# Performance work log

Measured on AMD Instinct MI355X. Metric: run time of the kernel, lower is better.

Reference implementation:

```python
import jax, jax.numpy as jnp
import numpy as np

B = 131072      # batch
IN = 1024       # input_dim
H = 384         # hidden[0]
L = 128         # latent_dim = hidden[1]
K = 32          # slots_k
R = 2           # top_r
TAU = 0.7


def setup_inputs() -> dict:
    key = jax.random.key(0)
    ks = jax.random.split(key, 8)
    s = 0.02
    f32 = jnp.float32
    return {
        "x":  jax.random.normal(ks[0], (B, IN), f32),
        "w1": jax.random.normal(ks[1], (IN, H), f32) * s,
        "b1": jnp.zeros((H,), f32),
        "w2": jax.random.normal(ks[2], (H, L), f32) * s,
        "b2": jnp.zeros((L,), f32),
        "mk": jax.random.normal(ks[3], (K, L), f32) * s,  # memory_keys
        "mv": jax.random.normal(ks[4], (K, L), f32) * s,  # memory_values
        "w3": jax.random.normal(ks[5], (2 * L, H), f32) * s,
        "b3": jnp.zeros((H,), f32),
        "w4": jax.random.normal(ks[6], (H, 1), f32) * s,
        "b4": jnp.zeros((1,), f32),
    }


def reference(x, w1, b1, w2, b2, mk, mv, w3, b3, w4, b4):
    # block_a: Linear -> GELU -> (Dropout=id in eval) -> Linear -> GELU
    z = jax.nn.gelu(x @ w1 + b1, approximate=False)
    z = jax.nn.gelu(z @ w2 + b2, approximate=False)          # [B, L]

    # top-r slot attention over memory bank
    logits = (z @ mk.T) / TAU                                 # [B, K]
    _, idx = jax.lax.top_k(logits, R)                         # [B, R]
    keep = jax.nn.one_hot(idx, K, dtype=logits.dtype).sum(-2) > 0  # [B, K] bool
    masked = jnp.where(keep, logits, -jnp.inf)
    attn = jax.nn.softmax(masked, axis=-1)                    # [B, K]
    mem = attn @ mv                                           # [B, L]

    fused = jnp.concatenate([z, mem], axis=-1)                # [B, 2L]

    # default head: Linear -> GELU -> Linear(.,1)
    h = jax.nn.gelu(fused @ w3 + b3, approximate=False)
    logit = (h @ w4 + b4)[..., 0]                             # [B]
    return jax.nn.sigmoid(logit)
```

## Files before the change

### kernel.cpp

```cpp
#include <hip/hip_runtime.h>

#define BATCH   131072
#define INDIM   1024
#define BM      64
#define BDIM    512
#define NBLK    (BATCH / BM)

#define WT_OFF   0
#define XT0_OFF  98304
#define XT1_OFF  114688
#define Z1_OFF   0
#define W2T0_OFF 50176
#define W2T1_OFF 58368
#define FZ_OFF   0
#define RP_OFF   33792
#define W3T0_OFF 42240
#define W3T1_OFF 66816
#define CB_OFF   131072
#define B1S_OFF  (CB_OFF)
#define B2S_OFF  (CB_OFF + 1536)
#define B3S_OFF  (CB_OFF + 2048)
#define W4S_OFF  (CB_OFF + 3584)
#define MKS_OFF  (CB_OFF + 5120)
#define SMEM_BYTES (CB_OFF + 13824)

typedef unsigned short u16;
typedef u16    u16x8  __attribute__((ext_vector_type(8)));
typedef u16    u16x4  __attribute__((ext_vector_type(4)));
typedef __bf16 bf16x8 __attribute__((ext_vector_type(8)));
typedef __bf16 bf16x4 __attribute__((ext_vector_type(4)));
typedef float  f32x4  __attribute__((ext_vector_type(4)));

__device__ __forceinline__ u16 f2bf(float f) {
  unsigned u = __float_as_uint(f);
  u += 0x7FFFu + ((u >> 16) & 1u);
  return (u16)(u >> 16);
}

__device__ __forceinline__ float gelu_fast(float v) {
  float t = v * v;
  float u = v * fmaf(t, 0.0356774081f, 0.7978845608f);
  float e = __builtin_amdgcn_exp2f(u * -2.885390082f);
  return v * __builtin_amdgcn_rcpf(1.0f + e);
}

__device__ __forceinline__ f32x4 mfma16(u16x8 a, u16x8 b, f32x4 c) {
  return __builtin_amdgcn_mfma_f32_16x16x32_bf16(
      __builtin_bit_cast(bf16x8, a), __builtin_bit_cast(bf16x8, b), c, 0, 0, 0);
}

__device__ __forceinline__ u16x8 cvt8(float4 a, float4 b) {
  bf16x8 r;
  r[0]=(__bf16)a.x; r[1]=(__bf16)a.y; r[2]=(__bf16)a.z; r[3]=(__bf16)a.w;
  r[4]=(__bf16)b.x; r[5]=(__bf16)b.y; r[6]=(__bf16)b.z; r[7]=(__bf16)b.w;
  return __builtin_bit_cast(u16x8, r);
}
__device__ __forceinline__ u16x4 cvt4(float4 a) {
  bf16x4 r;
  r[0]=(__bf16)a.x; r[1]=(__bf16)a.y; r[2]=(__bf16)a.z; r[3]=(__bf16)a.w;
  return __builtin_bit_cast(u16x4, r);
}

typedef __attribute__((address_space(3))) unsigned int       lds_u32;
typedef __attribute__((address_space(1))) const unsigned int glb_u32;
__device__ __forceinline__ void gload16(const void* g, void* l) {
  __builtin_amdgcn_global_load_lds((glb_u32*)g, (lds_u32*)l, 16, 0, 0);
}

#define FENCE_SCHED __builtin_amdgcn_sched_barrier(0)
#define SOFT_LGKM0 asm volatile("s_waitcnt lgkmcnt(0)" ::: "memory")
#define SOFT_VMN(N) asm volatile("s_waitcnt vmcnt(" #N ")" ::: "memory")
#define BARRIER_LGKM do { \
  asm volatile("s_waitcnt lgkmcnt(0)" ::: "memory"); \
  __builtin_amdgcn_s_barrier(); FENCE_SCHED; } while (0)

__global__ void prep_kernel(const float* __restrict__ w1, const float* __restrict__ w2,
                            const float* __restrict__ w3, u16* __restrict__ w1s,
                            u16* __restrict__ w2s, u16* __restrict__ w3s) {
  int i = blockIdx.x * 256 + threadIdx.x;
  if (i < 393216) {
    int t = i / 49152, p = i % 49152;
    int r = p >> 7, q = p & 127, cp = q >> 3, o = q & 7;
    int cs = (cp & 8) | ((cp ^ (r & 7)) & 7);
    int k = t * 128 + cs * 8 + o;
    w1s[i] = f2bf(w1[k * 384 + r]);
  } else if (i < 442368) {
    int j = i - 393216;
    int t = j / 4096, p = j % 4096;
    int r = p >> 5, q = p & 31, cp = q >> 3, o = q & 7;
    int k = t * 32 + ((cp ^ ((r >> 1) & 3)) << 3) + o;
    w2s[j] = f2bf(w2[k * 128 + r]);
  } else if (i < 540672) {
    int j = i - 442368;
    int t = j / 12288, p = j % 12288;
    int r = p >> 5, q = p & 31, cp = q >> 3, o = q & 7;
    int k = t * 32 + ((cp ^ ((r >> 1) & 3)) << 3) + o;
    w3s[j] = f2bf(w3[k * 384 + r]);
  }
}

__global__ __launch_bounds__(BDIM, 2) void fused_kernel(
    const float* __restrict__ x,  const u16* __restrict__ w1s,
    const float* __restrict__ b1, const u16* __restrict__ w2s,
    const float* __restrict__ b2, const float* __restrict__ mkw,
    const float* __restrict__ mvw, const u16* __restrict__ w3s,
    const float* __restrict__ b3, const float* __restrict__ w4,
    const float* __restrict__ b4, float* __restrict__ out) {
  extern __shared__ char smem[];
  u16*   z1  = (u16*)(smem + Z1_OFF);
  u16*   fz  = (u16*)(smem + FZ_OFF);
  float* b1s = (float*)(smem + B1S_OFF);
  float* b2s = (float*)(smem + B2S_OFF);
  float* b3s = (float*)(smem + B3S_OFF);
  float* w4s = (float*)(smem + W4S_OFF);
  u16*   mks = (u16*)(smem + MKS_OFF);
  float* rowpart = (float*)(smem + RP_OFF);

  const int tid  = threadIdx.x;
  const int lane = tid & 63;
  const int wid  = tid >> 6;
  const int l15  = lane & 15;
  const int g    = lane >> 4;
  const int swz4 = (l15 >> 1) & 3;
  const int row0 = blockIdx.x * BM;
  const int wrow = wid * 48;
  const int wstrip = wid * 6144;

  {
    const u16* ws = w1s + wstrip + lane * 8;
    u16* wd = (u16*)(smem + WT_OFF) + wstrip;
    #pragma unroll
    for (int i = 0; i < 12; ++i) gload16(ws + i * 512, wd + i * 512);
  }
  FENCE_SCHED;
  const int xrow = tid >> 3, xq = tid & 7;
  const float* xp = x + (long)(row0 + xrow) * INDIM + xq * 16;
  const int c0 = 2 * xq, c1 = 2 * xq + 1;
  const int s0 = ((c0 & 8) | ((c0 ^ (xrow & 7)) & 7)) * 8;
  const int s1 = ((c1 & 8) | ((c1 ^ (xrow & 7)) & 7)) * 8;
  float4 xa0 = *(const float4*)xp,        xa1 = *(const float4*)(xp + 4);
  float4 xb0 = *(const float4*)(xp + 8),  xb1 = *(const float4*)(xp + 12);

  if (tid < 384) b1s[tid] = b1[tid];
  if (tid < 128) b2s[tid] = b2[tid];
  if (tid < 384) b3s[tid] = b3[tid];
  if (tid < 384) w4s[tid] = w4[tid];
  {
    int r = tid >> 4, cc = (tid & 15) * 8;
    const float4* pm = (const float4*)(mkw + r * 128 + cc);
    *(u16x8*)(mks + r * 136 + cc) = cvt8(pm[0], pm[1]);
  }
  {
    u16* xb = (u16*)(smem + XT0_OFF) + xrow * 128;
    *(u16x8*)(xb + s0) = cvt8(xa0, xa1);
    *(u16x8*)(xb + s1) = cvt8(xb0, xb1);
  }
  {
    const float* p = xp + 128;
    xa0 = *(const float4*)p;       xa1 = *(const float4*)(p + 4);
    xb0 = *(const float4*)(p + 8); xb1 = *(const float4*)(p + 12);
  }
  BARRIER_LGKM;

  f32x4 acc[4][3];
  #pragma unroll
  for (int m = 0; m < 4; ++m)
    #pragma unroll
    for (int n = 0; n < 3; ++n) acc[m][n] = (f32x4){0.f, 0.f, 0.f, 0.f};

  const u16* wtb = (const u16*)(smem + WT_OFF);
  for (int kt = 0; kt < 8; ++kt) {
    if (kt < 7) { SOFT_VMN(4); } else { SOFT_VMN(0); }
    const u16* xtb = (const u16*)(smem + ((kt & 1) ? XT1_OFF : XT0_OFF));
    #pragma unroll
    for (int s = 0; s < 4; ++s) {
      const int c = s * 4 + g;
      const int cs = ((c & 8) | ((c ^ (l15 & 7)) & 7)) * 8;
      u16x8 af[4], bfr[3];
      #pragma unroll
      for (int m = 0; m < 4; ++m) af[m] = *(const u16x8*)(xtb + (m * 16 + l15) * 128 + cs);
      #pragma unroll
      for (int n = 0; n < 3; ++n) bfr[n] = *(const u16x8*)(wtb + (wrow + n * 16 + l15) * 128 + cs);
      #pragma unroll
      for (int m = 0; m < 4; ++m)
        #pragma unroll
        for (int n = 0; n < 3; ++n) acc[m][n] = mfma16(bfr[n], af[m], acc[m][n]);
    }
    SOFT_LGKM0;
    if (kt < 7) {
      {
        const u16* ws = w1s + (kt + 1) * 49152 + wstrip + lane * 8;
        u16* wd = (u16*)(smem + WT_OFF) + wstrip;
        #pragma unroll
        for (int i = 0; i < 12; ++i) gload16(ws + i * 512, wd + i * 512);
      }
      {
        u16* xb = (u16*)(smem + ((kt & 1) ? XT0_OFF : XT1_OFF)) + xrow * 128;
        *(u16x8*)(xb + s0) = cvt8(xa0, xa1);
        *(u16x8*)(xb + s1) = cvt8(xb0, xb1);
      }
      if (kt < 6) {
        const float* p = xp + (kt + 2) * 128;
        xa0 = *(const float4*)p;       xa1 = *(const float4*)(p + 4);
        xb0 = *(const float4*)(p + 8); xb1 = *(const float4*)(p + 12);
      }
    }
    BARRIER_LGKM;
  }

  {
    const u16* s2 = w2s + wid * 512 + lane * 8;
    gload16(s2, (u16*)(smem + W2T0_OFF) + wid * 512);
    const u16* s2b = w2s + 4096 + wid * 512 + lane * 8;
    gload16(s2b, (u16*)(smem + W2T1_OFF) + wid * 512);
  }
  #pragma unroll
  for (int m = 0; m < 4; ++m) {
    #pragma unroll
    for (int n = 0; n < 3; ++n) {
      int col = wrow + n * 16 + g * 4;
      float4 bv = *(const float4*)(b1s + col);
      f32x4 a = acc[m][n];
      float4 gv = {gelu_fast(a[0] + bv.x), gelu_fast(a[1] + bv.y),
                   gelu_fast(a[2] + bv.z), gelu_fast(a[3] + bv.w)};
      *(u16x4*)(z1 + (m * 16 + l15) * 392 + col) = cvt4(gv);
    }
  }
  BARRIER_LGKM;

  f32x4 acc2[4];
  #pragma unroll
  for (int m = 0; m < 4; ++m) acc2[m] = (f32x4){0.f, 0.f, 0.f, 0.f};
  for (int kt = 0; kt < 12; ++kt) {
    if (kt < 11) { SOFT_VMN(1); } else { SOFT_VMN(0); }
    const u16* wb = (const u16*)(smem + ((kt & 1) ? W2T1_OFF : W2T0_OFF));
    u16x8 a2f[4];
    #pragma unroll
    for (int m = 0; m < 4; ++m)
      a2f[m] = *(const u16x8*)(z1 + (m * 16 + l15) * 392 + kt * 32 + g * 8);
    u16x8 b2f = *(const u16x8*)(wb + (wid * 16 + l15) * 32 + (g ^ swz4) * 8);
    SOFT_LGKM0;
    if (kt < 10) {
      const u16* s2 = w2s + (kt + 2) * 4096 + wid * 512 + lane * 8;
      gload16(s2, (u16*)(smem + ((kt & 1) ? W2T1_OFF : W2T0_OFF)) + wid * 512);
    }
    #pragma unroll
    for (int m = 0; m < 4; ++m) acc2[m] = mfma16(b2f, a2f[m], acc2[m]);
  }
  BARRIER_LGKM;

  {
    const u16* s3 = w3s + wid * 1536 + lane * 8;
    u16* d3 = (u16*)(smem + W3T0_OFF) + wid * 1536;
    gload16(s3, d3); gload16(s3 + 512, d3 + 512); gload16(s3 + 1024, d3 + 1024);
    const u16* s3b = w3s + 12288 + wid * 1536 + lane * 8;
    u16* d3b = (u16*)(smem + W3T1_OFF) + wid * 1536;
    gload16(s3b, d3b); gload16(s3b + 512, d3b + 512); gload16(s3b + 1024, d3b + 1024);
  }
  #pragma unroll
  for (int m = 0; m < 4; ++m) {
    int col = wid * 16 + g * 4;
    float4 bv = *(const float4*)(b2s + col);
    f32x4 a = acc2[m];
    float4 gv = {gelu_fast(a[0] + bv.x), gelu_fast(a[1] + bv.y),
                 gelu_fast(a[2] + bv.z), gelu_fast(a[3] + bv.w)};
    *(u16x4*)(fz + (m * 16 + l15) * 264 + col) = cvt4(gv);
  }
  BARRIER_LGKM;

  if (wid < 4) {
    const int wr = wid * 16 + l15;
    f32x4 accl[2] = {(f32x4){0,0,0,0}, (f32x4){0,0,0,0}};
    #pragma unroll
    for (int ks = 0; ks < 4; ++ks) {
      u16x8 afz = *(const u16x8*)(fz + wr * 264 + ks * 32 + g * 8);
      u16x8 k0  = *(const u16x8*)(mks + l15 * 136 + ks * 32 + g * 8);
      u16x8 k1  = *(const u16x8*)(mks + (16 + l15) * 136 + ks * 32 + g * 8);
      accl[0] = mfma16(k0, afz, accl[0]);
      accl[1] = mfma16(k1, afz, accl[1]);
    }
    float m1 = -3.4e38f, m2 = -3.4e38f; int i1 = -1, i2 = -1;
    #pragma unroll
    for (int n = 0; n < 2; ++n)
      #pragma unroll
      for (int j = 0; j < 4; ++j) {
        float v = accl[n][j]; int idx = n * 16 + g * 4 + j;
        if (v > m1) { m2 = m1; i2 = i1; m1 = v; i1 = idx; }
        else if (v > m2) { m2 = v; i2 = idx; }
      }
    #pragma unroll
    for (int d = 16; d <= 32; d <<= 1) {
      float om1 = __shfl_xor(m1, d); int oi1 = __shfl_xor(i1, d);
      float om2 = __shfl_xor(m2, d); int oi2 = __shfl_xor(i2, d);
      bool take = (om1 > m1) || (om1 == m1 && oi1 < i1);
      if (take) {
        float nm2; int ni2;
        if (m1 > om2 || (m1 == om2 && i1 < oi2)) { nm2 = m1; ni2 = i1; }
        else { nm2 = om2; ni2 = oi2; }
        m1 = om1; i1 = oi1; m2 = nm2; i2 = ni2;
      } else {
        if (om1 > m2 || (om1 == m2 && oi1 < i2)) { m2 = om1; i2 = oi1; }
      }
    }
    float a1 = __builtin_amdgcn_rcpf(
        1.0f + __builtin_amdgcn_exp2f((m2 - m1) * (1.44269504f / 0.7f)));
    float a2 = 1.0f - a1;
    const float* v1 = mvw + i1 * 128 + g * 32;
    const float* v2 = mvw + i2 * 128 + g * 32;
    #pragma unroll
    for (int c = 0; c < 4; ++c) {
      float4 A0 = *(const float4*)(v1 + c * 8), A1 = *(const float4*)(v1 + c * 8 + 4);
      float4 B0 = *(const float4*)(v2 + c * 8), B1 = *(const float4*)(v2 + c * 8 + 4);
      float4 r0 = {a1*A0.x + a2*B0.x, a1*A0.y + a2*B0.y, a1*A0.z + a2*B0.z, a1*A0.w + a2*B0.w};
      float4 r1 = {a1*A1.x + a2*B1.x, a1*A1.y + a2*B1.y, a1*A1.z + a2*B1.z, a1*A1.w + a2*B1.w};
      *(u16x8*)(fz + wr * 264 + 128 + g * 32 + c * 8) = cvt8(r0, r1);
    }
  }
  BARRIER_LGKM;

  f32x4 acc3[4][3];
  #pragma unroll
  for (int m = 0; m < 4; ++m)
    #pragma unroll
    for (int n = 0; n < 3; ++n) acc3[m][n] = (f32x4){0.f, 0.f, 0.f, 0.f};
  for (int kt = 0; kt < 8; ++kt) {
    if (kt < 7) { SOFT_VMN(3); } else { SOFT_VMN(0); }
    const u16* wb = (const u16*)(smem + ((kt & 1) ? W3T1_OFF : W3T0_OFF));
    u16x8 a3f[4], b3f[3];
    #pragma unroll
    for (int m = 0; m < 4; ++m)
      a3f[m] = *(const u16x8*)(fz + (m * 16 + l15) * 264 + kt * 32 + g * 8);
    #pragma unroll
    for (int n = 0; n < 3; ++n)
      b3f[n] = *(const u16x8*)(wb + (wrow + n * 16 + l15) * 32 + (g ^ swz4) * 8);
    SOFT_LGKM0;
    if (kt < 6) {
      const u16* s3 = w3s + (kt + 2) * 12288 + wid * 1536 + lane * 8;
      u16* d3 = (u16*)(smem + ((kt & 1) ? W3T1_OFF : W3T0_OFF)) + wid * 1536;
      gload16(s3, d3); gload16(s3 + 512, d3 + 512); gload16(s3 + 1024, d3 + 1024);
    }
    #pragma unroll
    for (int m = 0; m < 4; ++m)
      #pragma unroll
      for (int n = 0; n < 3; ++n) acc3[m][n] = mfma16(b3f[n], a3f[m], acc3[m][n]);
  }

  #pragma unroll
  for (int m = 0; m < 4; ++m) {
    float s = 0.f;
    #pragma unroll
    for (int n = 0; n < 3; ++n) {
      int col = wrow + n * 16 + g * 4;
      float4 bv = *(const float4*)(b3s + col);
      float4 wv = *(const float4*)(w4s + col);
      f32x4 a = acc3[m][n];
      s += gelu_fast(a[0] + bv.x) * wv.x + gelu_fast(a[1] + bv.y) * wv.y +
           gelu_fast(a[2] + bv.z) * wv.z + gelu_fast(a[3] + bv.w) * wv.w;
    }
    s += __shfl_xor(s, 16);
    s += __shfl_xor(s, 32);
    if (lane < 16) rowpart[(m * 16 + l15) * 8 + wid] = s;
  }
  BARRIER_LGKM;
  if (tid < BM) {
    const float4* rp = (const float4*)(rowpart + tid * 8);
    float4 p0 = rp[0], p1 = rp[1];
    float lg = b4[0] + p0.x + p0.y + p0.z + p0.w + p1.x + p1.y + p1.z + p1.w;
    out[row0 + tid] = __builtin_amdgcn_rcpf(1.0f + __builtin_amdgcn_exp2f(-lg * 1.44269504f));
  }
}

extern "C" void kernel_launch(void* const* d_in, const int* in_sizes, int n_in,
                              void* d_out, int out_size, void* d_ws, size_t ws_size,
                              hipStream_t stream) {
  const float* x  = (const float*)d_in[0];
  const float* w1 = (const float*)d_in[1];
  const float* b1 = (const float*)d_in[2];
  const float* w2 = (const float*)d_in[3];
  const float* b2 = (const float*)d_in[4];
  const float* mk = (const float*)d_in[5];
  const float* mv = (const float*)d_in[6];
  const float* w3 = (const float*)d_in[7];
  const float* b3 = (const float*)d_in[8];
  const float* w4 = (const float*)d_in[9];
  const float* b4 = (const float*)d_in[10];

  u16* w1s = (u16*)d_ws;
  u16* w2s = w1s + 393216;
  u16* w3s = w1s + 442368;

  prep_kernel<<<2112, 256, 0, stream>>>(w1, w2, w3, w1s, w2s, w3s);

  (void)hipFuncSetAttribute(reinterpret_cast<const void*>(fused_kernel),
                            hipFuncAttributeMaxDynamicSharedMemorySize, SMEM_BYTES);
  fused_kernel<<<NBLK, BDIM, SMEM_BYTES, stream>>>(x, w1s, b1, w2s, b2, mk, mv, w3s,
                                                   b3, w4, b4, (float*)d_out);
}
```

Before: 279.7 us.

## Double batch tile to 128 rows with 2x4 wave grid and double-buffered W1

Raises the per-block row tile from 64 to 128 and splits the 8 waves into a 2x4 grid for the first GEMM, so each wave computes 64 rows by 96 columns. The W1 weight tile is cut to 64-wide K slices that are double-buffered in LDS, and the barrier sits mid-iteration so the next slice's loads overlap the MFMAs. The aim is to halve how often each block reloads the weights per row and to improve compute-to-load ratio. In exchange, accumulator register pressure doubles (24 plus 24 f32x4 tiles), which may hurt occupancy at 2 blocks/CU, and half as many blocks are launched.

```diff
diff --git a/kernel.cpp b/kernel.cpp
--- a/kernel.cpp
+++ b/kernel.cpp
@@ -2,20 +2,21 @@
 
 #define BATCH   131072
 #define INDIM   1024
-#define BM      64
+#define BM      128
 #define BDIM    512
 #define NBLK    (BATCH / BM)
 
-#define WT_OFF   0
+#define WT0_OFF  0
+#define WT1_OFF  49152
 #define XT0_OFF  98304
 #define XT1_OFF  114688
 #define Z1_OFF   0
-#define W2T0_OFF 50176
-#define W2T1_OFF 58368
+#define W2T0_OFF 100352
+#define W2T1_OFF 108544
 #define FZ_OFF   0
-#define RP_OFF   33792
-#define W3T0_OFF 42240
-#define W3T1_OFF 66816
+#define W3T0_OFF 67584
+#define W3T1_OFF 92160
+#define RP_OFF   116736
 #define CB_OFF   131072
 #define B1S_OFF  (CB_OFF)
 #define B2S_OFF  (CB_OFF + 1536)
@@ -79,10 +80,9 @@
                             u16* __restrict__ w2s, u16* __restrict__ w3s) {
   int i = blockIdx.x * 256 + threadIdx.x;
   if (i < 393216) {
-    int t = i / 49152, p = i % 49152;
-    int r = p >> 7, q = p & 127, cp = q >> 3, o = q & 7;
-    int cs = (cp & 8) | ((cp ^ (r & 7)) & 7);
-    int k = t * 128 + cs * 8 + o;
+    int t = i / 24576, p = i % 24576;
+    int r = p >> 6, q = p & 63, cp = q >> 3, o = q & 7;
+    int k = t * 64 + ((cp ^ (r & 7)) << 3) + o;
     w1s[i] = f2bf(w1[k * 384 + r]);
   } else if (i < 442368) {
     int j = i - 393216;
@@ -121,25 +121,32 @@
   const int wid  = tid >> 6;
   const int l15  = lane & 15;
   const int g    = lane >> 4;
+  const int sw   = l15 & 7;
   const int swz4 = (l15 >> 1) & 3;
   const int row0 = blockIdx.x * BM;
-  const int wrow = wid * 48;
-  const int wstrip = wid * 6144;
+  const int waveM = wid >> 2;
+  const int waveN = wid & 3;
+  const int wrow1 = waveN * 96;
+  const int wrow3 = wid * 48;
+  const int wstrip = wid * 3072;
 
   {
     const u16* ws = w1s + wstrip + lane * 8;
-    u16* wd = (u16*)(smem + WT_OFF) + wstrip;
-    #pragma unroll
-    for (int i = 0; i < 12; ++i) gload16(ws + i * 512, wd + i * 512);
+    u16* wd0 = (u16*)(smem + WT0_OFF) + wstrip;
+    #pragma unroll
+    for (int i = 0; i < 6; ++i) gload16(ws + i * 512, wd0 + i * 512);
+    const u16* ws1 = ws + 24576;
+    u16* wd1 = (u16*)(smem + WT1_OFF) + wstrip;
+    #pragma unroll
+    for (int i = 0; i < 6; ++i) gload16(ws1 + i * 512, wd1 + i * 512);
   }
   FENCE_SCHED;
-  const int xrow = tid >> 3, xq = tid & 7;
+  const int xrow = tid >> 2, xq = tid & 3;
   const float* xp = x + (long)(row0 + xrow) * INDIM + xq * 16;
-  const int c0 = 2 * xq, c1 = 2 * xq + 1;
-  const int s0 = ((c0 & 8) | ((c0 ^ (xrow & 7)) & 7)) * 8;
-  const int s1 = ((c1 & 8) | ((c1 ^ (xrow & 7)) & 7)) * 8;
-  float4 xa0 = *(const float4*)xp,        xa1 = *(const float4*)(xp + 4);
-  float4 xb0 = *(const float4*)(xp + 8),  xb1 = *(const float4*)(xp + 12);
+  const int xdst0 = xrow * 64 + (((2 * xq)     ^ (xrow & 7)) << 3);
+  const int xdst1 = xrow * 64 + (((2 * xq + 1) ^ (xrow & 7)) << 3);
+  float4 xa0 = *(const float4*)xp,       xa1 = *(const float4*)(xp + 4);
+  float4 xb0 = *(const float4*)(xp + 8), xb1 = *(const float4*)(xp + 12);
 
   if (tid < 384) b1s[tid] = b1[tid];
   if (tid < 128) b2s[tid] = b2[tid];
@@ -151,62 +158,68 @@
     *(u16x8*)(mks + r * 136 + cc) = cvt8(pm[0], pm[1]);
   }
   {
-    u16* xb = (u16*)(smem + XT0_OFF) + xrow * 128;
-    *(u16x8*)(xb + s0) = cvt8(xa0, xa1);
-    *(u16x8*)(xb + s1) = cvt8(xb0, xb1);
-  }
-  {
-    const float* p = xp + 128;
+    u16* xb = (u16*)(smem + XT0_OFF);
+    *(u16x8*)(xb + xdst0) = cvt8(xa0, xa1);
+    *(u16x8*)(xb + xdst1) = cvt8(xb0, xb1);
+  }
+  {
+    const float* p = xp + 64;
     xa0 = *(const float4*)p;       xa1 = *(const float4*)(p + 4);
     xb0 = *(const float4*)(p + 8); xb1 = *(const float4*)(p + 12);
   }
   BARRIER_LGKM;
 
-  f32x4 acc[4][3];
+  f32x4 acc[4][6];
   #pragma unroll
   for (int m = 0; m < 4; ++m)
     #pragma unroll
-    for (int n = 0; n < 3; ++n) acc[m][n] = (f32x4){0.f, 0.f, 0.f, 0.f};
-
-  const u16* wtb = (const u16*)(smem + WT_OFF);
-  for (int kt = 0; kt < 8; ++kt) {
-    if (kt < 7) { SOFT_VMN(4); } else { SOFT_VMN(0); }
+    for (int n = 0; n < 6; ++n) acc[m][n] = (f32x4){0.f, 0.f, 0.f, 0.f};
+
+  for (int kt = 0; kt < 16; ++kt) {
     const u16* xtb = (const u16*)(smem + ((kt & 1) ? XT1_OFF : XT0_OFF));
-    #pragma unroll
-    for (int s = 0; s < 4; ++s) {
-      const int c = s * 4 + g;
-      const int cs = ((c & 8) | ((c ^ (l15 & 7)) & 7)) * 8;
-      u16x8 af[4], bfr[3];
+    const u16* wtb = (const u16*)(smem + ((kt & 1) ? WT1_OFF : WT0_OFF));
+    u16x8 af[4], bfr[6];
+    const int c0 = (g ^ sw) * 8;
+    #pragma unroll
+    for (int m = 0; m < 4; ++m)
+      af[m] = *(const u16x8*)(xtb + (waveM * 64 + m * 16 + l15) * 64 + c0);
+    #pragma unroll
+    for (int n = 0; n < 6; ++n)
+      bfr[n] = *(const u16x8*)(wtb + (wrow1 + n * 16 + l15) * 64 + c0);
+    #pragma unroll
+    for (int m = 0; m < 4; ++m)
       #pragma unroll
-      for (int m = 0; m < 4; ++m) af[m] = *(const u16x8*)(xtb + (m * 16 + l15) * 128 + cs);
-      #pragma unroll
-      for (int n = 0; n < 3; ++n) bfr[n] = *(const u16x8*)(wtb + (wrow + n * 16 + l15) * 128 + cs);
-      #pragma unroll
-      for (int m = 0; m < 4; ++m)
+      for (int n = 0; n < 6; ++n) acc[m][n] = mfma16(bfr[n], af[m], acc[m][n]);
+    const int c1 = ((g + 4) ^ sw) * 8;
+    #pragma unroll
+    for (int m = 0; m < 4; ++m)
+      af[m] = *(const u16x8*)(xtb + (waveM * 64 + m * 16 + l15) * 64 + c1);
+    #pragma unroll
+    for (int n = 0; n < 6; ++n)
+      bfr[n] = *(const u16x8*)(wtb + (wrow1 + n * 16 + l15) * 64 + c1);
+    SOFT_LGKM0;
+    if (kt < 15) {
+      u16* xn = (u16*)(smem + ((kt & 1) ? XT0_OFF : XT1_OFF));
+      *(u16x8*)(xn + xdst0) = cvt8(xa0, xa1);
+      *(u16x8*)(xn + xdst1) = cvt8(xb0, xb1);
+      if (kt < 14) {
+        const u16* ws = w1s + (kt + 2) * 24576 + wstrip + lane * 8;
+        u16* wd = (u16*)(smem + ((kt & 1) ? WT1_OFF : WT0_OFF)) + wstrip;
         #pragma unroll
-        for (int n = 0; n < 3; ++n) acc[m][n] = mfma16(bfr[n], af[m], acc[m][n]);
-    }
-    SOFT_LGKM0;
-    if (kt < 7) {
-      {
-        const u16* ws = w1s + (kt + 1) * 49152 + wstrip + lane * 8;
-        u16* wd = (u16*)(smem + WT_OFF) + wstrip;
-        #pragma unroll
-        for (int i = 0; i < 12; ++i) gload16(ws + i * 512, wd + i * 512);
-      }
-      {
-        u16* xb = (u16*)(smem + ((kt & 1) ? XT0_OFF : XT1_OFF)) + xrow * 128;
-        *(u16x8*)(xb + s0) = cvt8(xa0, xa1);
-        *(u16x8*)(xb + s1) = cvt8(xb0, xb1);
-      }
-      if (kt < 6) {
-        const float* p = xp + (kt + 2) * 128;
+        for (int i = 0; i < 6; ++i) gload16(ws + i * 512, wd + i * 512);
+        FENCE_SCHED;
+        const float* p = xp + (kt + 2) * 64;
         xa0 = *(const float4*)p;       xa1 = *(const float4*)(p + 4);
         xb0 = *(const float4*)(p + 8); xb1 = *(const float4*)(p + 12);
       }
     }
-    BARRIER_LGKM;
-  }
+    #pragma unroll
+    for (int m = 0; m < 4; ++m)
+      #pragma unroll
+      for (int n = 0; n < 6; ++n) acc[m][n] = mfma16(bfr[n], af[m], acc[m][n]);
+    if (kt < 15) BARRIER_LGKM;
+  }
+  BARRIER_LGKM;
 
   {
     const u16* s2 = w2s + wid * 512 + lane * 8;
@@ -217,26 +230,26 @@
   #pragma unroll
   for (int m = 0; m < 4; ++m) {
     #pragma unroll
-    for (int n = 0; n < 3; ++n) {
-      int col = wrow + n * 16 + g * 4;
+    for (int n = 0; n < 6; ++n) {
+      int col = wrow1 + n * 16 + g * 4;
       float4 bv = *(const float4*)(b1s + col);
       f32x4 a = acc[m][n];
       float4 gv = {gelu_fast(a[0] + bv.x), gelu_fast(a[1] + bv.y),
                    gelu_fast(a[2] + bv.z), gelu_fast(a[3] + bv.w)};
-      *(u16x4*)(z1 + (m * 16 + l15) * 392 + col) = cvt4(gv);
-    }
-  }
-  BARRIER_LGKM;
-
-  f32x4 acc2[4];
-  #pragma unroll
-  for (int m = 0; m < 4; ++m) acc2[m] = (f32x4){0.f, 0.f, 0.f, 0.f};
+      *(u16x4*)(z1 + (waveM * 64 + m * 16 + l15) * 392 + col) = cvt4(gv);
+    }
+  }
+  BARRIER_LGKM;
+
+  f32x4 acc2[8];
+  #pragma unroll
+  for (int m = 0; m < 8; ++m) acc2[m] = (f32x4){0.f, 0.f, 0.f, 0.f};
   for (int kt = 0; kt < 12; ++kt) {
     if (kt < 11) { SOFT_VMN(1); } else { SOFT_VMN(0); }
     const u16* wb = (const u16*)(smem + ((kt & 1) ? W2T1_OFF : W2T0_OFF));
-    u16x8 a2f[4];
-    #pragma unroll
-    for (int m = 0; m < 4; ++m)
+    u16x8 a2f[8];
+    #pragma unroll
+    for (int m = 0; m < 8; ++m)
       a2f[m] = *(const u16x8*)(z1 + (m * 16 + l15) * 392 + kt * 32 + g * 8);
     u16x8 b2f = *(const u16x8*)(wb + (wid * 16 + l15) * 32 + (g ^ swz4) * 8);
     SOFT_LGKM0;
@@ -245,20 +258,20 @@
       gload16(s2, (u16*)(smem + ((kt & 1) ? W2T1_OFF : W2T0_OFF)) + wid * 512);
     }
     #pragma unroll
-    for (int m = 0; m < 4; ++m) acc2[m] = mfma16(b2f, a2f[m], acc2[m]);
-  }
-  BARRIER_LGKM;
-
-  {
-    const u16* s3 = w3s + wid * 1536 + lane * 8;
-    u16* d3 = (u16*)(smem + W3T0_OFF) + wid * 1536;
-    gload16(s3, d3); gload16(s3 + 512, d3 + 512); gload16(s3 + 1024, d3 + 1024);
+    for (int m = 0; m < 8; ++m) acc2[m] = mfma16(b2f, a2f[m], acc2[m]);
+  }
+  BARRIER_LGKM;
+
+  {
+    const u16* s3 = w3s + wrow3 * 32 + lane * 8;
+    u16* d30 = (u16*)(smem + W3T0_OFF) + wid * 1536;
+    gload16(s3, d30); gload16(s3 + 512, d30 + 512); gload16(s3 + 1024, d30 + 1024);
     const u16* s3b = w3s + 12288 + wid * 1536 + lane * 8;
-    u16* d3b = (u16*)(smem + W3T1_OFF) + wid * 1536;
-    gload16(s3b, d3b); gload16(s3b + 512, d3b + 512); gload16(s3b + 1024, d3b + 1024);
-  }
-  #pragma unroll
-  for (int m = 0; m < 4; ++m) {
+    u16* d31 = (u16*)(smem + W3T1_OFF) + wid * 1536;
+    gload16(s3b, d31); gload16(s3b + 512, d31 + 512); gload16(s3b + 1024, d31 + 1024);
+  }
+  #pragma unroll
+  for (int m = 0; m < 8; ++m) {
     int col = wid * 16 + g * 4;
     float4 bv = *(const float4*)(b2s + col);
     f32x4 a = acc2[m];
@@ -268,7 +281,7 @@
   }
   BARRIER_LGKM;
 
-  if (wid < 4) {
+  {
     const int wr = wid * 16 + l15;
     f32x4 accl[2] = {(f32x4){0,0,0,0}, (f32x4){0,0,0,0}};
     #pragma unroll
@@ -318,21 +331,21 @@
   }
   BARRIER_LGKM;
 
-  f32x4 acc3[4][3];
-  #pragma unroll
-  for (int m = 0; m < 4; ++m)
+  f32x4 acc3[8][3];
+  #pragma unroll
+  for (int m = 0; m < 8; ++m)
     #pragma unroll
     for (int n = 0; n < 3; ++n) acc3[m][n] = (f32x4){0.f, 0.f, 0.f, 0.f};
   for (int kt = 0; kt < 8; ++kt) {
     if (kt < 7) { SOFT_VMN(3); } else { SOFT_VMN(0); }
     const u16* wb = (const u16*)(smem + ((kt & 1) ? W3T1_OFF : W3T0_OFF));
-    u16x8 a3f[4], b3f[3];
-    #pragma unroll
-    for (int m = 0; m < 4; ++m)
+    u16x8 a3f[8], b3f[3];
+    #pragma unroll
+    for (int m = 0; m < 8; ++m)
       a3f[m] = *(const u16x8*)(fz + (m * 16 + l15) * 264 + kt * 32 + g * 8);
     #pragma unroll
     for (int n = 0; n < 3; ++n)
-      b3f[n] = *(const u16x8*)(wb + (wrow + n * 16 + l15) * 32 + (g ^ swz4) * 8);
+      b3f[n] = *(const u16x8*)(wb + (wrow3 + n * 16 + l15) * 32 + (g ^ swz4) * 8);
     SOFT_LGKM0;
     if (kt < 6) {
       const u16* s3 = w3s + (kt + 2) * 12288 + wid * 1536 + lane * 8;
@@ -340,17 +353,17 @@
       gload16(s3, d3); gload16(s3 + 512, d3 + 512); gload16(s3 + 1024, d3 + 1024);
     }
     #pragma unroll
-    for (int m = 0; m < 4; ++m)
+    for (int m = 0; m < 8; ++m)
       #pragma unroll
       for (int n = 0; n < 3; ++n) acc3[m][n] = mfma16(b3f[n], a3f[m], acc3[m][n]);
   }
 
   #pragma unroll
-  for (int m = 0; m < 4; ++m) {
+  for (int m = 0; m < 8; ++m) {
     float s = 0.f;
     #pragma unroll
     for (int n = 0; n < 3; ++n) {
-      int col = wrow + n * 16 + g * 4;
+      int col = wrow3 + n * 16 + g * 4;
       float4 bv = *(const float4*)(b3s + col);
       float4 wv = *(const float4*)(w4s + col);
       f32x4 a = acc3[m][n];
```

Result: faster. 230.4 us (-17.6%).
